# Performance work log

Measured on AMD Instinct MI355X. Metric: run time of the kernel, lower is better.

Reference implementation:

```python
import jax, jax.numpy as jnp
import numpy as np

D_CUT = 5.0   # cosine-cutoff distance
SIZE = 128    # rbf size == hidden_channels (nn_dist size = in_channels)
L = 2         # num_layers
EPS = 0.0     # GIN eps (non-trainable, initial 0)


def _rbf(d):
    # d: (E,) distances -> (E, SIZE) expnorm RBF with cosine cutoff
    d = d[:, None]
    start = float(np.exp(-D_CUT))
    means = jnp.linspace(start, 1.0, SIZE)
    beta = (2.0 / SIZE * (1.0 - start)) ** (-2)
    dc = jnp.minimum(d, D_CUT)
    cutoff = 0.5 * (jnp.cos(dc * jnp.pi / D_CUT) + 1.0)
    return cutoff * jnp.exp(-beta * (jnp.exp(-d) - means) ** 2)


def setup_inputs() -> dict:
    key = jax.random.key(0)
    ks = jax.random.split(key, 40)
    it = iter(range(40))
    def k():
        return ks[next(it)]
    N, H, ED, AS = 100000, 128, 4, 4
    def w(shape, s):
        return jax.random.normal(k(), shape, jnp.float32) * s
    inp = {}
    inp['x_lig'] = jax.random.normal(k(), (N, H), jnp.float32)
    inp['x_pock'] = jax.random.normal(k(), (N, H), jnp.float32)
    for name, E in (('bond', 200000), ('lp', 400000), ('pl', 400000)):
        inp['ei_' + name] = jax.random.randint(k(), (2, E), 0, N, jnp.int32)
        inp['ew_' + name] = jax.random.uniform(k(), (E,), jnp.float32) * D_CUT
        inp['ea_' + name] = jax.random.normal(k(), (E, AS), jnp.float32)
    inp['W0'] = w((3, AS, ED), 0.5)                 # initial per-edge-type lins (no bias)
    inp['Wd'] = w((L, 3, H, 2 * H), H ** -0.5)      # RBFDistanceScaleShift lin
    inp['bd'] = jnp.zeros((L, 3, 2 * H), jnp.float32)
    inp['We'] = w((L, 3, ED, H), 0.5)               # EGINConv.lin (edge_dim -> hidden)
    inp['be'] = jnp.zeros((L, 3, H), jnp.float32)
    inp['W1'] = w((L, 3, H, H), H ** -0.5)          # nn_node MLP layer 1
    inp['b1'] = jnp.zeros((L, 3, H), jnp.float32)
    inp['W2'] = w((L, 3, H, H), H ** -0.5)          # nn_node MLP layer 2
    inp['b2'] = jnp.zeros((L, 3, H), jnp.float32)
    return inp


def reference(x_lig, x_pock, ei_bond, ew_bond, ea_bond, ei_lp, ew_lp, ea_lp,
              ei_pl, ew_pl, ea_pl, W0, Wd, bd, We, be, W1, b1, W2, b2):
    # HeteroEGIN.forward: initial per-edge-type linear on raw edge attrs (bias-free)
    ea0 = ea_bond @ W0[0]
    ea1 = ea_lp @ W0[1]
    ea2 = ea_pl @ W0[2]

    def conv(x_src, x_dst, ei, ew, ea, t, l):
        # EGINConv per edge type t, layer l
        ss = _rbf(ew) @ Wd[l, t] + bd[l, t]            # (E, 2H) scale/shift from distance
        scale, shift = jnp.split(ss, 2, axis=1)
        xj = x_src[ei[0]] + (ea @ We[l, t] + be[l, t])  # gather + edge-attr lin
        msg = jax.nn.relu(xj * scale + shift)           # gated message
        agg = jax.ops.segment_sum(msg, ei[1], num_segments=x_dst.shape[0])
        o = agg + (1.0 + EPS) * x_dst
        return jax.nn.relu(o @ W1[l, t] + b1[l, t]) @ W2[l, t] + b2[l, t]

    for l in range(L):
        # to_hetero: sum conv outputs across edge types per destination node type
        new_lig = (conv(x_lig, x_lig, ei_bond, ew_bond, ea0, 0, l)
                   + conv(x_pock, x_lig, ei_pl, ew_pl, ea2, 2, l))
        new_pock = conv(x_lig, x_pock, ei_lp, ew_lp, ea1, 1, l)
        if l < L - 1:  # BasicGNN: act between layers, none after last (jk=None)
            new_lig = jax.nn.relu(new_lig)
            new_pock = jax.nn.relu(new_pock)
        x_lig, x_pock = new_lig, new_pock
    return jnp.concatenate([x_lig, x_pock], axis=0)
```

## Files before the change

### kernel.cpp

```cpp
#include <hip/hip_runtime.h>
#include <hip/hip_bf16.h>
#include <hip/hip_fp16.h>
#include <cmath>

typedef __attribute__((ext_vector_type(8))) short short8_t;
typedef __attribute__((ext_vector_type(4))) float f32x4;

static __device__ __forceinline__ short f2bs(float f) {
    union { __hip_bfloat16 h; short s; } u;
    u.h = __float2bfloat16(f);
    return u.s;
}
static __device__ __forceinline__ float bs2f(unsigned int us) {
    union { float f; unsigned int i; } u;
    u.i = us << 16;
    return u.f;
}
static __device__ __forceinline__ unsigned int pack2bf(float a, float b) {
    return (unsigned int)(unsigned short)f2bs(a) |
           ((unsigned int)(unsigned short)f2bs(b) << 16);
}
static __device__ __forceinline__ void lds_barrier() {
    asm volatile("s_waitcnt lgkmcnt(0)\n\ts_barrier" ::: "memory");
}

__global__ void pack_kernel(const float* __restrict__ Wd,
                            const float* __restrict__ W1,
                            const float* __restrict__ W2,
                            const float* __restrict__ W0,
                            const float* __restrict__ We,
                            short* __restrict__ pWd,
                            short* __restrict__ pW1,
                            short* __restrict__ pW2,
                            float* __restrict__ Mb)
{
    const int tid = blockIdx.x * blockDim.x + threadIdx.x;
    const int stride = gridDim.x * blockDim.x;
    for (int i = tid; i < 6 * 32768; i += stride) {
        int c = i >> 15, rem = i & 32767;
        int f = rem >> 9, l = (rem >> 3) & 63, j = rem & 7;
        int kk = f >> 4, nt = f & 15;
        int k = kk * 32 + (l >> 4) * 8 + j;
        int n = nt * 16 + (l & 15);
        pWd[i] = f2bs(Wd[(size_t)c * 32768 + k * 256 + n]);
    }
    for (int i = tid; i < 6 * 16384; i += stride) {
        int c = i >> 14, rem = i & 16383;
        int f = rem >> 9, l = (rem >> 3) & 63, j = rem & 7;
        int kk = f >> 3, nt = f & 7;
        int k = kk * 32 + (l >> 4) * 8 + j;
        int n = nt * 16 + (l & 15);
        pW1[i] = f2bs(W1[(size_t)c * 16384 + k * 128 + n]);
        pW2[i] = f2bs(W2[(size_t)c * 16384 + k * 128 + n]);
    }
    for (int i = tid; i < 6 * 512; i += stride) {
        int c = i >> 9, rem = i & 511;
        int a = rem >> 7, h = rem & 127;
        int t = c % 3;
        float m = 0.f;
        #pragma unroll
        for (int j = 0; j < 4; ++j)
            m = fmaf(W0[t * 16 + a * 4 + j], We[(size_t)c * 512 + j * 128 + h], m);
        Mb[i] = m;
    }
}

__global__ void tobf16_kernel(const float* __restrict__ a, const float* __restrict__ b,
                              unsigned short* __restrict__ oa, unsigned short* __restrict__ ob,
                              int n4)
{
    int i = blockIdx.x * blockDim.x + threadIdx.x;
    const int stride = gridDim.x * blockDim.x;
    for (; i < n4; i += stride) {
        float4 va = ((const float4*)a)[i];
        uint2 pa; pa.x = pack2bf(va.x, va.y); pa.y = pack2bf(va.z, va.w);
        ((uint2*)oa)[i] = pa;
        float4 vb = ((const float4*)b)[i];
        uint2 pb; pb.x = pack2bf(vb.x, vb.y); pb.y = pack2bf(vb.z, vb.w);
        ((uint2*)ob)[i] = pb;
    }
}

__global__ void hist_kernel(const int* __restrict__ ei, int* __restrict__ cnt, int E)
{
    for (int e = blockIdx.x * blockDim.x + threadIdx.x; e < E;
         e += gridDim.x * blockDim.x)
        atomicAdd(&cnt[ei[E + e]], 1);
}

__global__ void scan1k_kernel(int* __restrict__ data, int* __restrict__ bsum, int n)
{
    __shared__ int buf[1024];
    const int gid = blockIdx.x * 1024 + threadIdx.x;
    int v = (gid < n) ? data[gid] : 0;
    buf[threadIdx.x] = v;
    __syncthreads();
    for (int off = 1; off < 1024; off <<= 1) {
        int t = (threadIdx.x >= off) ? buf[threadIdx.x - off] : 0;
        __syncthreads();
        buf[threadIdx.x] += t;
        __syncthreads();
    }
    if (gid < n) data[gid] = buf[threadIdx.x] - v;
    if (bsum && threadIdx.x == 1023) bsum[blockIdx.x] = buf[1023];
}

__global__ void scan_add_kernel(int* __restrict__ data, const int* __restrict__ bsum,
                                int* __restrict__ cursor, int n)
{
    const int gid = blockIdx.x * 1024 + threadIdx.x;
    if (gid < n) {
        int v = data[gid] + bsum[blockIdx.x];
        data[gid] = v;
        cursor[gid] = v;
    }
}

__global__ void scatter_kernel(const int* __restrict__ ei, const float* __restrict__ ew,
                               const float4* __restrict__ ea, int* __restrict__ cursor,
                               float* __restrict__ ewp, float4* __restrict__ eap,
                               int* __restrict__ srcp, int* __restrict__ dstp, int E)
{
    for (int e = blockIdx.x * blockDim.x + threadIdx.x; e < E;
         e += gridDim.x * blockDim.x) {
        int d = ei[E + e];
        int p = atomicAdd(&cursor[d], 1);
        ewp[p]  = ew[e];
        eap[p]  = ea[e];
        srcp[p] = ei[e];
        dstp[p] = d;
    }
}

__global__ __launch_bounds__(512, 2)
void edge_mfma_kernel(
    const unsigned short* __restrict__ xsb,
    const int* __restrict__ srcp, const int* __restrict__ dstp,
    const float* __restrict__ ewp, const float4* __restrict__ eap,
    const short* __restrict__ pWd, const float* __restrict__ bd,
    const float* __restrict__ Mb, const float* __restrict__ be,
    __half2* __restrict__ agg, int E, int ntiles,
    float rs, float rstep, float rbeta)
{
    __shared__ short sRbf[64 * 128];
    __shared__ __half sSS[64 * 256];

    const int t = threadIdx.x;
    const int lane = t & 63;
    const int w = t >> 6;
    const int l15 = lane & 15;
    const int l4 = lane >> 4;

    short8_t bfrag[4][2];
    #pragma unroll
    for (int kk = 0; kk < 4; ++kk)
        #pragma unroll
        for (int i = 0; i < 2; ++i)
            bfrag[kk][i] = *(const short8_t*)&pWd[((kk * 16 + 2 * w + i) * 64 + lane) * 8];
    float bdv[2];
    #pragma unroll
    for (int i = 0; i < 2; ++i) bdv[i] = bd[(2 * w + i) * 16 + l15];
    const float be0 = be[2 * lane], be1 = be[2 * lane + 1];
    float ma0[4], ma1[4];
    #pragma unroll
    for (int a = 0; a < 4; ++a) {
        ma0[a] = Mb[a * 128 + 2 * lane];
        ma1[a] = Mb[a * 128 + 2 * lane + 1];
    }

    const int stride = gridDim.x;
    int tile = blockIdx.x;
    if (tile >= ntiles) return;

    float dd_c; int dst_c; float4 ea_c;
    unsigned int gx[8];
    {
        const int e0 = tile << 6;
        int eL = e0 + lane;
        int eLc = eL < E ? eL : E - 1;
        dd_c = ewp[eLc];
        int es = e0 + w * 8 + (lane & 7);
        int esv = es < E ? es : E - 1;
        dst_c = (es < E) ? dstp[esv] : -1;
        int src_c = srcp[esv];
        ea_c = eap[esv];
        #pragma unroll
        for (int r = 0; r < 8; ++r) {
            int srn = __shfl(src_c, r);
            gx[r] = *(const unsigned int*)&xsb[(size_t)srn * 128 + lane * 2];
        }
    }

    for (; tile < ntiles; tile += stride) {
        const float edv = __expf(-dd_c);
        const float dcc = fminf(dd_c, 5.0f);
        const float cutv = 0.5f * (__cosf(dcc * 0.62831853071795864769f) + 1.0f);
        {
            char* base = (char*)sRbf + lane * 256;
            #pragma unroll
            for (int c = 0; c < 2; ++c) {
                short8_t v;
                #pragma unroll
                for (int j = 0; j < 8; ++j) {
                    float mean = rs + (float)(w * 16 + c * 8 + j) * rstep;
                    float diff = edv - mean;
                    v[j] = f2bs(cutv * __expf(-rbeta * diff * diff));
                }
                *(short8_t*)(base + ((w * 32 + c * 16) ^ ((lane & 7) << 4))) = v;
            }
        }
        unsigned int xjr[8];
        #pragma unroll
        for (int r = 0; r < 8; ++r) {
            float ea0 = __shfl(ea_c.x, r), ea1 = __shfl(ea_c.y, r);
            float ea2 = __shfl(ea_c.z, r), ea3 = __shfl(ea_c.w, r);
            unsigned int g = gx[r];
            float x0 = bs2f(g & 0xffffu), x1 = bs2f(g >> 16);
            float o0 = x0 + be0 + ea0 * ma0[0] + ea1 * ma0[1] + ea2 * ma0[2] + ea3 * ma0[3];
            float o1 = x1 + be1 + ea0 * ma1[0] + ea1 * ma1[1] + ea2 * ma1[2] + ea3 * ma1[3];
            xjr[r] = pack2bf(o0, o1);
        }

        lds_barrier();

        const int ntile = tile + stride;
        const bool has_next = ntile < ntiles;
        float dd_n = 0.f; int dst_n = -1; int src_n = 0;
        float4 ea_n = {0.f, 0.f, 0.f, 0.f};
        if (has_next) {
            const int e0n = ntile << 6;
            int eL = e0n + lane;
            int eLc = eL < E ? eL : E - 1;
            dd_n = ewp[eLc];
            int es = e0n + w * 8 + (lane & 7);
            int esv = es < E ? es : E - 1;
            dst_n = (es < E) ? dstp[esv] : -1;
            src_n = srcp[esv];
            ea_n = eap[esv];
        }
        __builtin_amdgcn_sched_barrier(0);

        f32x4 acc[4][2];
        #pragma unroll
        for (int m = 0; m < 4; ++m) {
            acc[m][0] = (f32x4){0.f, 0.f, 0.f, 0.f};
            acc[m][1] = (f32x4){0.f, 0.f, 0.f, 0.f};
        }
        #pragma unroll
        for (int kk = 0; kk < 4; ++kk) {
            short8_t af[4];
            #pragma unroll
            for (int m = 0; m < 4; ++m) {
                int row = m * 16 + l15;
                int byte = row * 256 + ((kk * 64 + l4 * 16) ^ ((row & 7) << 4));
                af[m] = *(const short8_t*)((const char*)sRbf + byte);
            }
            #pragma unroll
            for (int m = 0; m < 4; ++m)
                #pragma unroll
                for (int i = 0; i < 2; ++i)
                    acc[m][i] = __builtin_amdgcn_mfma_f32_16x16x32_bf16(
                        af[m], bfrag[kk][i], acc[m][i], 0, 0, 0);
        }

        #pragma unroll
        for (int m = 0; m < 4; ++m)
            #pragma unroll
            for (int i = 0; i < 2; ++i) {
                int col = (2 * w + i) * 16 + l15;
                #pragma unroll
                for (int r = 0; r < 4; ++r) {
                    int row = m * 16 + l4 * 4 + r;
                    int byte = row * 512 + ((col * 2) ^ ((row & 7) << 4));
                    *(__half*)((char*)sSS + byte) = __float2half(acc[m][i][r] + bdv[i]);
                }
            }

        if (has_next) {
            #pragma unroll
            for (int r = 0; r < 8; ++r) {
                int srn = __shfl(src_n, r);
                gx[r] = *(const unsigned int*)&xsb[(size_t)srn * 128 + lane * 2];
            }
        }
        const int dst_f = dst_c;
        dd_c = dd_n; dst_c = dst_n; ea_c = ea_n;

        lds_barrier();

        {
            float a0 = 0.f, a1 = 0.f;
            int rdst = __shfl(dst_f, 0);
            #pragma unroll
            for (int r = 0; r < 8; ++r) {
                int e = 8 * w + r;
                unsigned int sc = *(const unsigned int*)
                    ((const char*)sSS + e * 512 + ((lane * 4) ^ ((e & 7) << 4)));
                unsigned int sh = *(const unsigned int*)
                    ((const char*)sSS + e * 512 + ((256 + lane * 4) ^ ((e & 7) << 4)));
                float2 scf = __half22float2(*(const __half2*)&sc);
                float2 shf = __half22float2(*(const __half2*)&sh);
                unsigned int g = xjr[r];
                float x0 = bs2f(g & 0xffffu), x1 = bs2f(g >> 16);
                float m0 = fmaxf(fmaf(x0, scf.x, shf.x), 0.0f);
                float m1 = fmaxf(fmaf(x1, scf.y, shf.y), 0.0f);
                int d = __shfl(dst_f, r);
                if (d != rdst) {
                    if (rdst >= 0) {
                        __half2 hv = __floats2half2_rn(a0, a1);
                        unsigned int hb;
                        __builtin_memcpy(&hb, &hv, 4);
                        if (hb)
                            unsafeAtomicAdd(agg + (size_t)rdst * 64 + lane, hv);
                    }
                    a0 = 0.f; a1 = 0.f; rdst = d;
                }
                a0 += m0; a1 += m1;
            }
            if (rdst >= 0) {
                __half2 hv = __floats2half2_rn(a0, a1);
                unsigned int hb;
                __builtin_memcpy(&hb, &hv, 4);
                if (hb)
                    unsafeAtomicAdd(agg + (size_t)rdst * 64 + lane, hv);
            }
        }
    }
}

__global__ __launch_bounds__(256)
void node_mfma_kernel(
    const __half2* __restrict__ agg,
    const float* __restrict__ xdf, const unsigned short* __restrict__ xdb,
    const short* __restrict__ pW1, const float* __restrict__ b1,
    const short* __restrict__ pW2, const float* __restrict__ b2,
    float* __restrict__ outf, unsigned short* __restrict__ outb,
    int N, int ntiles, int accumulate, int relu_out)
{
    __shared__ short sA[64 * 128];
    __shared__ short sH[64 * 128];

    const int t = threadIdx.x;
    const int lane = t & 63;
    const int w = t >> 6;
    const int l15 = lane & 15;
    const int l4 = lane >> 4;

    short8_t w1f[4][2], w2f[4][2];
    #pragma unroll
    for (int kk = 0; kk < 4; ++kk)
        #pragma unroll
        for (int p = 0; p < 2; ++p) {
            int nt = 2 * w + p;
            w1f[kk][p] = *(const short8_t*)&pW1[((kk * 8 + nt) * 64 + lane) * 8];
            w2f[kk][p] = *(const short8_t*)&pW2[((kk * 8 + nt) * 64 + lane) * 8];
        }
    float b1v[2], b2v[2];
    #pragma unroll
    for (int p = 0; p < 2; ++p) {
        int col = (2 * w + p) * 16 + l15;
        b1v[p] = b1[col];
        b2v[p] = b2[col];
    }

    for (int tile = blockIdx.x; tile < ntiles; tile += gridDim.x) {
        const int n0 = tile << 6;
        #pragma unroll
        for (int i = 0; i < 4; ++i) {
            int idx = i * 256 + t;
            int row = idx >> 4, c8 = idx & 15;
            int gr = n0 + row; if (gr >= N) gr = N - 1;
            union { float4 f; __half2 h[4]; } ar;
            ar.f = ((const float4*)agg)[(size_t)gr * 16 + c8];
            float xv[8];
            if (xdf) {
                float4 x0 = ((const float4*)xdf)[(size_t)gr * 32 + c8 * 2];
                float4 x1 = ((const float4*)xdf)[(size_t)gr * 32 + c8 * 2 + 1];
                xv[0] = x0.x; xv[1] = x0.y; xv[2] = x0.z; xv[3] = x0.w;
                xv[4] = x1.x; xv[5] = x1.y; xv[6] = x1.z; xv[7] = x1.w;
            } else {
                uint4 xr = ((const uint4*)xdb)[(size_t)gr * 16 + c8];
                xv[0] = bs2f(xr.x & 0xffffu); xv[1] = bs2f(xr.x >> 16);
                xv[2] = bs2f(xr.y & 0xffffu); xv[3] = bs2f(xr.y >> 16);
                xv[4] = bs2f(xr.z & 0xffffu); xv[5] = bs2f(xr.z >> 16);
                xv[6] = bs2f(xr.w & 0xffffu); xv[7] = bs2f(xr.w >> 16);
            }
            short8_t v;
            #pragma unroll
            for (int j = 0; j < 4; ++j) {
                float2 a2 = __half22float2(ar.h[j]);
                v[2 * j]     = f2bs(a2.x + xv[2 * j]);
                v[2 * j + 1] = f2bs(a2.y + xv[2 * j + 1]);
            }
            int byte = row * 256 + ((c8 * 16) ^ ((row & 7) << 4));
            *(short8_t*)((char*)sA + byte) = v;
        }
        lds_barrier();

        f32x4 acc[4][2];
        #pragma unroll
        for (int m = 0; m < 4; ++m) {
            acc[m][0] = (f32x4){0.f, 0.f, 0.f, 0.f};
            acc[m][1] = (f32x4){0.f, 0.f, 0.f, 0.f};
        }
        #pragma unroll
        for (int kk = 0; kk < 4; ++kk) {
            short8_t af[4];
            #pragma unroll
            for (int m = 0; m < 4; ++m) {
                int row = m * 16 + l15;
                int byte = row * 256 + ((kk * 64 + l4 * 16) ^ ((row & 7) << 4));
                af[m] = *(const short8_t*)((const char*)sA + byte);
            }
            #pragma unroll
            for (int m = 0; m < 4; ++m)
                #pragma unroll
                for (int p = 0; p < 2; ++p)
                    acc[m][p] = __builtin_amdgcn_mfma_f32_16x16x32_bf16(
                        af[m], w1f[kk][p], acc[m][p], 0, 0, 0);
        }
        #pragma unroll
        for (int m = 0; m < 4; ++m)
            #pragma unroll
            for (int p = 0; p < 2; ++p) {
                int col = (2 * w + p) * 16 + l15;
                #pragma unroll
                for (int r = 0; r < 4; ++r) {
                    int row = m * 16 + l4 * 4 + r;
                    short hs = f2bs(fmaxf(acc[m][p][r] + b1v[p], 0.f));
                    int byte = row * 256 + ((col * 2) ^ ((row & 7) << 4));
                    *(short*)((char*)sH + byte) = hs;
                }
            }
        lds_barrier();

        f32x4 acc2[4][2];
        #pragma unroll
        for (int m = 0; m < 4; ++m) {
            acc2[m][0] = (f32x4){0.f, 0.f, 0.f, 0.f};
            acc2[m][1] = (f32x4){0.f, 0.f, 0.f, 0.f};
        }
        #pragma unroll
        for (int kk = 0; kk < 4; ++kk) {
            short8_t af[4];
            #pragma unroll
            for (int m = 0; m < 4; ++m) {
                int row = m * 16 + l15;
                int byte = row * 256 + ((kk * 64 + l4 * 16) ^ ((row & 7) << 4));
                af[m] = *(const short8_t*)((const char*)sH + byte);
            }
            #pragma unroll
            for (int m = 0; m < 4; ++m)
                #pragma unroll
                for (int p = 0; p < 2; ++p)
                    acc2[m][p] = __builtin_amdgcn_mfma_f32_16x16x32_bf16(
                        af[m], w2f[kk][p], acc2[m][p], 0, 0, 0);
        }
        #pragma unroll
        for (int m = 0; m < 4; ++m)
            #pragma unroll
            for (int p = 0; p < 2; ++p) {
                int col = (2 * w + p) * 16 + l15;
                #pragma unroll
                for (int r = 0; r < 4; ++r) {
                    int row = n0 + m * 16 + l4 * 4 + r;
                    if (row < N) {
                        float v = acc2[m][p][r] + b2v[p];
                        if (outf) {
                            float* op = &outf[(size_t)row * 128 + col];
                            if (accumulate) v += *op;
                            if (relu_out) v = fmaxf(v, 0.f);
                            *op = v;
                        } else {
                            unsigned short* op = &outb[(size_t)row * 128 + col];
                            if (accumulate) v += bs2f((unsigned int)*op);
                            if (relu_out) v = fmaxf(v, 0.f);
                            *op = (unsigned short)f2bs(v);
                        }
                    }
                }
            }
    }
}

extern "C" void kernel_launch(void* const* d_in, const int* in_sizes, int n_in,
                              void* d_out, int out_size, void* d_ws, size_t ws_size,
                              hipStream_t stream)
{
    const float* x_lig   = (const float*)d_in[0];
    const float* x_pock  = (const float*)d_in[1];
    const int*   ei_bond = (const int*)d_in[2];
    const float* ew_bond = (const float*)d_in[3];
    const float* ea_bond = (const float*)d_in[4];
    const int*   ei_lp   = (const int*)d_in[5];
    const float* ew_lp   = (const float*)d_in[6];
    const float* ea_lp   = (const float*)d_in[7];
    const int*   ei_pl   = (const int*)d_in[8];
    const float* ew_pl   = (const float*)d_in[9];
    const float* ea_pl   = (const float*)d_in[10];
    const float* W0 = (const float*)d_in[11];
    const float* Wd = (const float*)d_in[12];
    const float* bd = (const float*)d_in[13];
    const float* We = (const float*)d_in[14];
    const float* be = (const float*)d_in[15];
    const float* W1 = (const float*)d_in[16];
    const float* b1 = (const float*)d_in[17];
    const float* W2 = (const float*)d_in[18];
    const float* b2 = (const float*)d_in[19];

    const int H = 128;
    const int N = in_sizes[0] / H;
    const int E_bond = in_sizes[3];
    const int E_lp   = in_sizes[6];
    const int E_pl   = in_sizes[9];

    char* wp = (char*)d_ws;
    auto alloc = [&](size_t bytes) -> char* {
        char* r = wp;
        wp += (bytes + 255) & ~(size_t)255;
        return r;
    };
    unsigned short* A   = (unsigned short*)alloc((size_t)N * H * 2);
    unsigned short* Bb  = (unsigned short*)alloc((size_t)N * H * 2);
    unsigned short* C   = (unsigned short*)alloc((size_t)N * H * 2);
    __half*  agg  = (__half*)alloc((size_t)N * H * 2);
    float4*  eapB = (float4*)alloc((size_t)E_bond * 16);
    float4*  eapL = (float4*)alloc((size_t)E_lp * 16);
    float4*  eapP = (float4*)alloc((size_t)E_pl * 16);
    float*   ewpB = (float*)alloc((size_t)E_bond * 4);
    float*   ewpL = (float*)alloc((size_t)E_lp * 4);
    float*   ewpP = (float*)alloc((size_t)E_pl * 4);
    int*     srcB = (int*)alloc((size_t)E_bond * 4);
    int*     srcL = (int*)alloc((size_t)E_lp * 4);
    int*     srcP = (int*)alloc((size_t)E_pl * 4);
    int*     dstB = (int*)alloc((size_t)E_bond * 4);
    int*     dstL = (int*)alloc((size_t)E_lp * 4);
    int*     dstP = (int*)alloc((size_t)E_pl * 4);
    short*   pWd  = (short*)alloc(6 * 32768 * 2);
    short*   pW1s = (short*)alloc(6 * 16384 * 2);
    short*   pW2s = (short*)alloc(6 * 16384 * 2);
    float*   Mb   = (float*)alloc(6 * 512 * 4);
    int*     cnt    = (int*)alloc((size_t)N * 4);
    int*     cursor = (int*)alloc((size_t)N * 4);
    int*     bsum   = (int*)alloc(1024 * 4);

    float* outL = (float*)d_out;
    float* outP = outL + (size_t)N * H;

    const int capE = 2 * 256;
    const int capN = 4 * 256;

    tobf16_kernel<<<512, 256, 0, stream>>>(x_lig, x_pock, A, Bb, N * H / 4);
    pack_kernel<<<256, 256, 0, stream>>>(Wd, W1, W2, W0, We, pWd, pW1s, pW2s, Mb);

    const int nb = (N + 1023) / 1024;
    auto sortset = [&](const int* ei_, const float* ew_, const float* ea_, int E,
                       float* ewp, float4* eap, int* sr716, int* dstp) {
        hipMemsetAsync(cnt, 0, (size_t)N * sizeof(int), stream);
        hist_kernel<<<512, 256, 0, stream>>>(ei_, cnt, E);
        scan1k_kernel<<<nb, 1024, 0, stream>>>(cnt, bsum, N);
        scan1k_kernel<<<1, 1024, 0, stream>>>(bsum, nullptr, nb);
        scan_add_kernel<<<nb, 1024, 0, stream>>>(cnt, bsum, cursor, N);
        scatter_kernel<<<512, 256, 0, stream>>>(ei_, ew_, (const float4*)ea_,
                                                cursor, ewp, eap, sr716, dstp, E);
    };
    sortset(ei_bond, ew_bond, ea_bond, E_bond, ewpB, eapB, srcB, dstB);
    sortset(ei_lp,   ew_lp,   ea_lp,   E_lp,   ewpL, eapL, srcL, dstL);
    sortset(ei_pl,   ew_pl,   ea_pl,   E_pl,   ewpP, eapP, srcP, dstP);

    const double start_d = exp(-5.0);
    const float rs    = (float)start_d;
    const float rstep = (float)((1.0 - start_d) / 127.0);
    const float rbeta = (float)std::pow(2.0 / 128.0 * (1.0 - start_d), -2.0);

    auto conv = [&](const unsigned short* src,
                    const float* xdf, const unsigned short* xdb,
                    const int* srcp, const int* dstp, const float* ewp,
                    const float4* eap, int E,
                    int l, int tt, float* outf, unsigned short* outb,
                    int accum, int relu) {
        hipMemsetAsync(agg, 0, (size_t)N * H * sizeof(__half), stream);
        const int lt = l * 3 + tt;
        const int ntE = (E + 63) / 64;
        const int gE = ntE < capE ? ntE : capE;
        edge_mfma_kernel<<<gE, 512, 0, stream>>>(
            src, srcp, dstp, ewp, eap,
            pWd + (size_t)lt * 32768, bd + (size_t)lt * 256,
            Mb + (size_t)lt * 512, be + (size_t)lt * 128,
            (__half2*)agg, E, ntE, rs, rstep, rbeta);
        const int ntN = (N + 63) / 64;
        const int gN = ntN < capN ? ntN : capN;
        node_mfma_kernel<<<gN, 256, 0, stream>>>(
            (const __half2*)agg, xdf, xdb,
            pW1s + (size_t)lt * 16384, b1 + (size_t)lt * 128,
            pW2s + (size_t)lt * 16384, b2 + (size_t)lt * 128,
            outf, outb, N, ntN, accum, relu);
    };

    conv(A,  x_pock, nullptr, srcL, dstL, ewpL, eapL, E_lp,   0, 1, nullptr, C, 0, 1);
    conv(A,  x_lig,  nullptr, srcB, dstB, ewpB, eapB, E_bond, 0, 0, nullptr, A, 0, 0);
    conv(Bb, x_lig,  nullptr, srcP, dstP, ewpP, eapP, E_pl,   0, 2, nullptr, A, 1, 1);
    conv(A, nullptr, A, srcB, dstB, ewpB, eapB, E_bond, 1, 0, outL, nullptr, 0, 0);
    conv(C, nullptr, A, srcP, dstP, ewpP, eapP, E_pl,   1, 2, outL, nullptr, 1, 0);
    conv(A, nullptr, C, srcL, dstL, ewpL, eapL, E_lp,   1, 1, outP, nullptr, 0, 0);
}
```

Baseline: 936.2 us.

## Pack edge records into uint4, zero agg in node kernel, halve edge grid

Each edge's src, dst and edge attributes, with the attributes converted to bf16, are packed into one 16-byte record so the edge kernel issues a single coalesced load per lane instead of several array loads. Records are then distributed to waves by shuffle. The node kernel zeroes each agg row after reading it, which removes the per-conv memset; a single memset now runs up front. The edge kernel grid cap drops from 512 to 256 blocks. Costs: bf16 rounding of the edge attributes, and a change in work distribution.

After: 849.7 us. 1.1x faster.

```diff
diff --git a/kernel.cpp b/kernel.cpp
--- a/kernel.cpp
+++ b/kernel.cpp
@@ -118,25 +118,28 @@
 
 __global__ void scatter_kernel(const int* __restrict__ ei, const float* __restrict__ ew,
                                const float4* __restrict__ ea, int* __restrict__ cursor,
-                               float* __restrict__ ewp, float4* __restrict__ eap,
-                               int* __restrict__ srcp, int* __restrict__ dstp, int E)
+                               uint4* __restrict__ rec, float* __restrict__ ewp, int E)
 {
     for (int e = blockIdx.x * blockDim.x + threadIdx.x; e < E;
          e += gridDim.x * blockDim.x) {
         int d = ei[E + e];
         int p = atomicAdd(&cursor[d], 1);
-        ewp[p]  = ew[e];
-        eap[p]  = ea[e];
-        srcp[p] = ei[e];
-        dstp[p] = d;
+        float4 a = ea[e];
+        uint4 r;
+        r.x = (unsigned int)ei[e];
+        r.y = (unsigned int)d;
+        r.z = pack2bf(a.x, a.y);
+        r.w = pack2bf(a.z, a.w);
+        rec[p] = r;
+        ewp[p] = ew[e];
     }
 }
 
 __global__ __launch_bounds__(512, 2)
 void edge_mfma_kernel(
     const unsigned short* __restrict__ xsb,
-    const int* __restrict__ srcp, const int* __restrict__ dstp,
-    const float* __restrict__ ewp, const float4* __restrict__ eap,
+    const uint4* __restrict__ rec,
+    const float* __restrict__ ewp,
     const short* __restrict__ pWd, const float* __restrict__ bd,
     const float* __restrict__ Mb, const float* __restrict__ be,
     __half2* __restrict__ agg, int E, int ntiles,
@@ -172,28 +175,26 @@
     int tile = blockIdx.x;
     if (tile >= ntiles) return;
 
-    float dd_c; int dst_c; float4 ea_c;
+    float ew_c; int src_c, dst_c; unsigned int ea01_c, ea23_c;
     unsigned int gx[8];
     {
-        const int e0 = tile << 6;
-        int eL = e0 + lane;
-        int eLc = eL < E ? eL : E - 1;
-        dd_c = ewp[eLc];
-        int es = e0 + w * 8 + (lane & 7);
-        int esv = es < E ? es : E - 1;
-        dst_c = (es < E) ? dstp[esv] : -1;
-        int src_c = srcp[esv];
-        ea_c = eap[esv];
-        #pragma unroll
-        for (int r = 0; r < 8; ++r) {
-            int srn = __shfl(src_c, r);
-            gx[r] = *(const unsigned int*)&xsb[(size_t)srn * 128 + lane * 2];
+        int eL = (tile << 6) + lane;
+        int ec = eL < E ? eL : E - 1;
+        uint4 r = rec[ec];
+        ew_c = ewp[ec];
+        src_c = (int)r.x;
+        dst_c = (eL < E) ? (int)r.y : -1;
+        ea01_c = r.z; ea23_c = r.w;
+        #pragma unroll
+        for (int rr = 0; rr < 8; ++rr) {
+            int srn = __shfl(src_c, 8 * w + rr);
+            gx[rr] = *(const unsigned int*)&xsb[(size_t)srn * 128 + lane * 2];
         }
     }
 
     for (; tile < ntiles; tile += stride) {
-        const float edv = __expf(-dd_c);
-        const float dcc = fminf(dd_c, 5.0f);
+        const float edv = __expf(-ew_c);
+        const float dcc = fminf(ew_c, 5.0f);
         const float cutv = 0.5f * (__cosf(dcc * 0.62831853071795864769f) + 1.0f);
         {
             char* base = (char*)sRbf + lane * 256;
@@ -212,8 +213,10 @@
         unsigned int xjr[8];
         #pragma unroll
         for (int r = 0; r < 8; ++r) {
-            float ea0 = __shfl(ea_c.x, r), ea1 = __shfl(ea_c.y, r);
-            float ea2 = __shfl(ea_c.z, r), ea3 = __shfl(ea_c.w, r);
+            unsigned int a01 = __shfl(ea01_c, 8 * w + r);
+            unsigned int a23 = __shfl(ea23_c, 8 * w + r);
+            float ea0 = bs2f(a01 & 0xffffu), ea1 = bs2f(a01 >> 16);
+            float ea2 = bs2f(a23 & 0xffffu), ea3 = bs2f(a23 >> 16);
             unsigned int g = gx[r];
             float x0 = bs2f(g & 0xffffu), x1 = bs2f(g >> 16);
             float o0 = x0 + be0 + ea0 * ma0[0] + ea1 * ma0[1] + ea2 * ma0[2] + ea3 * ma0[3];
@@ -225,18 +228,16 @@
 
         const int ntile = tile + stride;
         const bool has_next = ntile < ntiles;
-        float dd_n = 0.f; int dst_n = -1; int src_n = 0;
-        float4 ea_n = {0.f, 0.f, 0.f, 0.f};
+        float ew_n = 0.f; int src_n = 0, dst_n = -1;
+        unsigned int ea01_n = 0, ea23_n = 0;
         if (has_next) {
-            const int e0n = ntile << 6;
-            int eL = e0n + lane;
-            int eLc = eL < E ? eL : E - 1;
-            dd_n = ewp[eLc];
-            int es = e0n + w * 8 + (lane & 7);
-            int esv = es < E ? es : E - 1;
-            dst_n = (es < E) ? dstp[esv] : -1;
-            src_n = srcp[esv];
-            ea_n = eap[esv];
+            int eL = (ntile << 6) + lane;
+            int ec = eL < E ? eL : E - 1;
+            uint4 r = rec[ec];
+            ew_n = ewp[ec];
+            src_n = (int)r.x;
+            dst_n = (eL < E) ? (int)r.y : -1;
+            ea01_n = r.z; ea23_n = r.w;
         }
         __builtin_amdgcn_sched_barrier(0);
 
@@ -279,18 +280,18 @@
         if (has_next) {
             #pragma unroll
             for (int r = 0; r < 8; ++r) {
-                int srn = __shfl(src_n, r);
+                int srn = __shfl(src_n, 8 * w + r);
                 gx[r] = *(const unsigned int*)&xsb[(size_t)srn * 128 + lane * 2];
             }
         }
         const int dst_f = dst_c;
-        dd_c = dd_n; dst_c = dst_n; ea_c = ea_n;
+        ew_c = ew_n; src_c = src_n; dst_c = dst_n; ea01_c = ea01_n; ea23_c = ea23_n;
 
         lds_barrier();
 
         {
             float a0 = 0.f, a1 = 0.f;
-            int rdst = __shfl(dst_f, 0);
+            int rdst = __shfl(dst_f, 8 * w);
             #pragma unroll
             for (int r = 0; r < 8; ++r) {
                 int e = 8 * w + r;
@@ -304,7 +305,7 @@
                 float x0 = bs2f(g & 0xffffu), x1 = bs2f(g >> 16);
                 float m0 = fmaxf(fmaf(x0, scf.x, shf.x), 0.0f);
                 float m1 = fmaxf(fmaf(x1, scf.y, shf.y), 0.0f);
-                int d = __shfl(dst_f, r);
+                int d = __shfl(dst_f, e);
                 if (d != rdst) {
                     if (rdst >= 0) {
                         __half2 hv = __floats2half2_rn(a0, a1);
@@ -330,7 +331,7 @@
 
 __global__ __launch_bounds__(256)
 void node_mfma_kernel(
-    const __half2* __restrict__ agg,
+    __half2* __restrict__ agg,
     const float* __restrict__ xdf, const unsigned short* __restrict__ xdb,
     const short* __restrict__ pW1, const float* __restrict__ b1,
     const short* __restrict__ pW2, const float* __restrict__ b2,
@@ -363,6 +364,8 @@
         b2v[p] = b2[col];
     }
 
+    const float4 zero4 = {0.f, 0.f, 0.f, 0.f};
+
     for (int tile = blockIdx.x; tile < ntiles; tile += gridDim.x) {
         const int n0 = tile << 6;
         #pragma unroll
@@ -372,6 +375,7 @@
             int gr = n0 + row; if (gr >= N) gr = N - 1;
             union { float4 f; __half2 h[4]; } ar;
             ar.f = ((const float4*)agg)[(size_t)gr * 16 + c8];
+            ((float4*)agg)[(size_t)gr * 16 + c8] = zero4;
             float xv[8];
             if (xdf) {
                 float4 x0 = ((const float4*)xdf)[(size_t)gr * 32 + c8 * 2];
@@ -524,18 +528,12 @@
     unsigned short* Bb  = (unsigned short*)alloc((size_t)N * H * 2);
     unsigned short* C   = (unsigned short*)alloc((size_t)N * H * 2);
     __half*  agg  = (__half*)alloc((size_t)N * H * 2);
-    float4*  eapB = (float4*)alloc((size_t)E_bond * 16);
-    float4*  eapL = (float4*)alloc((size_t)E_lp * 16);
-    float4*  eapP = (float4*)alloc((size_t)E_pl * 16);
+    uint4*   recB = (uint4*)alloc((size_t)E_bond * 16);
+    uint4*   recL = (uint4*)alloc((size_t)E_lp * 16);
+    uint4*   recP = (uint4*)alloc((size_t)E_pl * 16);
     float*   ewpB = (float*)alloc((size_t)E_bond * 4);
     float*   ewpL = (float*)alloc((size_t)E_lp * 4);
     float*   ewpP = (float*)alloc((size_t)E_pl * 4);
-    int*     srcB = (int*)alloc((size_t)E_bond * 4);
-    int*     srcL = (int*)alloc((size_t)E_lp * 4);
-    int*     srcP = (int*)alloc((size_t)E_pl * 4);
-    int*     dstB = (int*)alloc((size_t)E_bond * 4);
-    int*     dstL = (int*)alloc((size_t)E_lp * 4);
-    int*     dstP = (int*)alloc((size_t)E_pl * 4);
     short*   pWd  = (short*)alloc(6 * 32768 * 2);
     short*   pW1s = (short*)alloc(6 * 16384 * 2);
     short*   pW2s = (short*)alloc(6 * 16384 * 2);
@@ -547,26 +545,27 @@
     float* outL = (float*)d_out;
     float* outP = outL + (size_t)N * H;
 
-    const int capE = 2 * 256;
+    const int capE = 256;
     const int capN = 4 * 256;
 
+    hipMemsetAsync(agg, 0, (size_t)N * H * sizeof(__half), stream);
     tobf16_kernel<<<512, 256, 0, stream>>>(x_lig, x_pock, A, Bb, N * H / 4);
     pack_kernel<<<256, 256, 0, stream>>>(Wd, W1, W2, W0, We, pWd, pW1s, pW2s, Mb);
 
     const int nb = (N + 1023) / 1024;
     auto sortset = [&](const int* ei_, const float* ew_, const float* ea_, int E,
-                       float* ewp, float4* eap, int* sr716, int* dstp) {
+                       uint4* rec, float* ewp) {
         hipMemsetAsync(cnt, 0, (size_t)N * sizeof(int), stream);
         hist_kernel<<<512, 256, 0, stream>>>(ei_, cnt, E);
         scan1k_kernel<<<nb, 1024, 0, stream>>>(cnt, bsum, N);
         scan1k_kernel<<<1, 1024, 0, stream>>>(bsum, nullptr, nb);
         scan_add_kernel<<<nb, 1024, 0, stream>>>(cnt, bsum, cursor, N);
         scatter_kernel<<<512, 256, 0, stream>>>(ei_, ew_, (const float4*)ea_,
-                                                cursor, ewp, eap, sr716, dstp, E);
+                                                cursor, rec, ewp, E);
     };
-    sortset(ei_bond, ew_bond, ea_bond, E_bond, ewpB, eapB, srcB, dstB);
-    sortset(ei_lp,   ew_lp,   ea_lp,   E_lp,   ewpL, eapL, srcL, dstL);
-    sortset(ei_pl,   ew_pl,   ea_pl,   E_pl,   ewpP, eapP, srcP, dstP);
+    sortset(ei_bond, ew_bond, ea_bond, E_bond, recB, ewpB);
+    sortset(ei_lp,   ew_lp,   ea_lp,   E_lp,   recL, ewpL);
+    sortset(ei_pl,   ew_pl,   ea_pl,   E_pl,   recP, ewpP);
 
     const double start_d = exp(-5.0);
     const float rs    = (float)start_d;
@@ -575,32 +574,30 @@
 
     auto conv = [&](const unsigned short* src,
                     const float* xdf, const unsigned short* xdb,
-                    const int* srcp, const int* dstp, const float* ewp,
-                    const float4* eap, int E,
+                    const uint4* rec, const float* ewp, int E,
                     int l, int tt, float* outf, unsigned short* outb,
                     int accum, int relu) {
-        hipMemsetAsync(agg, 0, (size_t)N * H * sizeof(__half), stream);
         const int lt = l * 3 + tt;
         const int ntE = (E + 63) / 64;
         const int gE = ntE < capE ? ntE : capE;
         edge_mfma_kernel<<<gE, 512, 0, stream>>>(
-            src, srcp, dstp, ewp, eap,
+            src, rec, ewp,
             pWd + (size_t)lt * 32768, bd + (size_t)lt * 256,
             Mb + (size_t)lt * 512, be + (size_t)lt * 128,
             (__half2*)agg, E, ntE, rs, rstep, rbeta);
         const int ntN = (N + 63) / 64;
         const int gN = ntN < capN ? ntN : capN;
         node_mfma_kernel<<<gN, 256, 0, stream>>>(
-            (const __half2*)agg, xdf, xdb,
+            (__half2*)agg, xdf, xdb,
             pW1s + (size_t)lt * 16384, b1 + (size_t)lt * 128,
             pW2s + (size_t)lt * 16384, b2 + (size_t)lt * 128,
             outf, outb, N, ntN, accum, relu);
     };
 
-    conv(A,  x_pock, nullptr, srcL, dstL, ewpL, eapL, E_lp,   0, 1, nullptr, C, 0, 1);
-    conv(A,  x_lig,  nullptr, srcB, dstB, ewpB, eapB, E_bond, 0, 0, nullptr, A, 0, 0);
-    conv(Bb, x_lig,  nullptr, srcP, dstP, ewpP, eapP, E_pl,   0, 2, nullptr, A, 1, 1);
-    conv(A, nullptr, A, srcB, dstB, ewpB, eapB, E_bond, 1, 0, outL, nullptr, 0, 0);
-    conv(C, nullptr, A, srcP, dstP, ewpP, eapP, E_pl,   1, 2, outL, nullptr, 1, 0);
-    conv(A, nullptr, C, srcL, dstL, ewpL, eapL, E_lp,   1, 1, outP, nullptr, 0, 0);
-}
+    conv(A,  x_pock, nullptr, recL, ewpL, E_lp,   0, 1, nullptr, C, 0, 1);
+    conv(A,  x_lig,  nullptr, recB, ewpB, E_bond, 0, 0, nullptr, A, 0, 0);
+    conv(Bb, x_lig,  nullptr, recP, ewpP, E_pl,   0, 2, nullptr, A, 1, 1);
+    conv(A, nullptr, A, recB, ewpB, E_bond, 1, 0, outL, nullptr, 0, 0);
+    conv(C, nullptr, A, recP, ewpP, E_pl,   1, 2, outL, nullptr, 1, 0);
+    conv(A, nullptr, C, recL, ewpL, E_lp,   1, 1, outP, nullptr, 0, 0);
+}
```
